# Kernel tuning notes

Hardware: AMD Instinct MI355X
Metric: run time of the kernel (lower is better)

## Reference

```python
import jax, jax.numpy as jnp
import numpy as np

N = 100000
E = 600000
H = 128
EPS = 1e-5


def _layer_norm(x, g, b):
    m = jnp.mean(x, axis=-1, keepdims=True)
    v = jnp.var(x, axis=-1, keepdims=True)
    return (x - m) * jax.lax.rsqrt(v + EPS) * g + b


def _mlp_ln(x, ws, bs, g, b):
    # Linear->ReLU x3, Linear, LayerNorm
    for i in range(4):
        x = x @ ws[i] + bs[i]
        if i < 3:
            x = jax.nn.relu(x)
    return _layer_norm(x, g, b)


def setup_inputs():
    key = jax.random.key(0)
    ks = jax.random.split(key, 32)

    def w(k, i, o):
        return jax.random.normal(k, (i, o), jnp.float32) * (1.0 / np.sqrt(i))

    inp = {
        "node_attr": jax.random.normal(ks[0], (N, H), jnp.float32),
        "edge_attr": jax.random.normal(ks[1], (E, H), jnp.float32),
        "edge_index": jax.random.randint(ks[2], (2, E), 0, N, jnp.int32),
        "num_nodes": N,
        # edge MLP: 3H -> H -> H -> H -> H, LayerNorm(H)
        "ew0": w(ks[3], 3 * H, H), "eb0": jnp.zeros((H,), jnp.float32),
        "ew1": w(ks[4], H, H),     "eb1": jnp.zeros((H,), jnp.float32),
        "ew2": w(ks[5], H, H),     "eb2": jnp.zeros((H,), jnp.float32),
        "ew3": w(ks[6], H, H),     "eb3": jnp.zeros((H,), jnp.float32),
        "eg": jnp.ones((H,), jnp.float32), "ebt": jnp.zeros((H,), jnp.float32),
        # node MLP: 2H -> H -> H -> H -> H, LayerNorm(H)
        "nw0": w(ks[7], 2 * H, H), "nb0": jnp.zeros((H,), jnp.float32),
        "nw1": w(ks[8], H, H),     "nb1": jnp.zeros((H,), jnp.float32),
        "nw2": w(ks[9], H, H),     "nb2": jnp.zeros((H,), jnp.float32),
        "nw3": w(ks[10], H, H),    "nb3": jnp.zeros((H,), jnp.float32),
        "ng": jnp.ones((H,), jnp.float32), "nbt": jnp.zeros((H,), jnp.float32),
    }
    return inp


def reference(node_attr, edge_attr, edge_index, num_nodes,
              ew0, eb0, ew1, eb1, ew2, eb2, ew3, eb3, eg, ebt,
              nw0, nb0, nw1, nb1, nw2, nb2, nw3, nb3, ng, nbt):
    senders, receivers = edge_index[0], edge_index[1]

    # EdgeBlock: gather, concat, MLP+LN
    collected_edges = jnp.concatenate(
        [node_attr[senders], node_attr[receivers], edge_attr], axis=1)  # [E, 3H]
    updated_edge = _mlp_ln(collected_edges, [ew0, ew1, ew2, ew3],
                           [eb0, eb1, eb2, eb3], eg, ebt)  # [E, H]

    # NodeBlock: scatter_add over receivers, concat, MLP+LN
    agg = jax.ops.segment_sum(updated_edge, receivers, num_segments=num_nodes)  # [N, H]
    collected_nodes = jnp.concatenate([node_attr, agg], axis=-1)  # [N, 2H]
    updated_node = _mlp_ln(collected_nodes, [nw0, nw1, nw2, nw3],
                           [nb0, nb1, nb2, nb3], ng, nbt)  # [N, H]

    # residual connections
    return (updated_node + node_attr, updated_edge + edge_attr)
```

## Files before the change

### kernel.cpp

```cpp
#include <hip/hip_runtime.h>

#define HN 128
#define NNODES 100000
#define NEDGES 600000

typedef __attribute__((ext_vector_type(8))) short short8;
typedef __attribute__((ext_vector_type(4))) float f32x4;

__device__ __forceinline__ unsigned short f2bf(float x) {
    unsigned u = __float_as_uint(x);
    u += 0x7FFFu + ((u >> 16) & 1u);
    return (unsigned short)(u >> 16);
}
__device__ __forceinline__ float bf2f(unsigned short h) {
    return __uint_as_float(((unsigned)h) << 16);
}

__device__ __forceinline__ f32x4 mfma16(short8 a, short8 b, f32x4 c) {
    return __builtin_amdgcn_mfma_f32_16x16x32_bf16(a, b, c, 0, 0, 0);
}

__device__ __forceinline__ void split_frag(const float xs[8], short8 &hi, short8 &lo) {
    #pragma unroll
    for (int e = 0; e < 8; ++e) {
        unsigned short h = f2bf(xs[e]);
        hi[e] = (short)h;
        lo[e] = (short)f2bf(xs[e] - bf2f(h));
    }
}

__device__ __forceinline__ void load_frags_global(const float* __restrict__ row,
                                                  short8 ahi[4], short8 alo[4], int g) {
    #pragma unroll
    for (int t = 0; t < 4; ++t) {
        float4 v0 = *(const float4*)(row + 32*t + 8*g);
        float4 v1 = *(const float4*)(row + 32*t + 8*g + 4);
        float xs[8] = {v0.x, v0.y, v0.z, v0.w, v1.x, v1.y, v1.z, v1.w};
        split_frag(xs, ahi[t], alo[t]);
    }
}

__device__ __forceinline__ void mlp_layer2(f32x4 C[2][8],
                                           const short8 ahi[2][4], const short8 alo[2][4],
                                           const unsigned short* __restrict__ Whi,
                                           const unsigned short* __restrict__ Wlo,
                                           int mat, int lane) {
    #pragma unroll
    for (int t = 0; t < 4; ++t) {
        #pragma unroll
        for (int n = 0; n < 8; ++n) {
            size_t idx = ((size_t)((mat*32 + t*8 + n)*64 + lane)) * 8;
            short8 bh = *(const short8*)(Whi + idx);
            short8 bl = *(const short8*)(Wlo + idx);
            #pragma unroll
            for (int i = 0; i < 2; ++i) {
                f32x4 a = C[i][n];
                a = mfma16(ahi[i][t], bh, a);
                a = mfma16(ahi[i][t], bl, a);
                a = mfma16(alo[i][t], bh, a);
                C[i][n] = a;
            }
        }
    }
}

__device__ __forceinline__ void c_to_lds(float* buf, const f32x4 C[8], int g, int c) {
    #pragma unroll
    for (int n = 0; n < 8; ++n) {
        #pragma unroll
        for (int j = 0; j < 4; ++j) {
            int row = 4*g + j;
            int col = 16*n + c;
            buf[(row*HN + col) ^ ((row & 7) << 2)] = C[n][j];
        }
    }
}
__device__ __forceinline__ void lds_to_frags(const float* buf, short8 ahi[4], short8 alo[4],
                                             int g, int c) {
    #pragma unroll
    for (int t = 0; t < 4; ++t) {
        int w0 = c*HN + 32*t + 8*g;
        int x  = (c & 7) << 2;
        float4 v0 = *(const float4*)(buf + (w0 ^ x));
        float4 v1 = *(const float4*)(buf + ((w0 + 4) ^ x));
        float xs[8] = {v0.x, v0.y, v0.z, v0.w, v1.x, v1.y, v1.z, v1.w};
        split_frag(xs, ahi[t], alo[t]);
    }
}

__device__ __forceinline__ void add_bias_act(f32x4 C[8], const float* __restrict__ b,
                                             int c, bool do_relu) {
    #pragma unroll
    for (int n = 0; n < 8; ++n) {
        float bv = b[16*n + c];
        #pragma unroll
        for (int j = 0; j < 4; ++j) {
            float v = C[n][j] + bv;
            C[n][j] = do_relu ? fmaxf(v, 0.0f) : v;
        }
    }
}

__device__ __forceinline__ void apply_ln(f32x4 C[8], const float* __restrict__ gamma,
                                         const float* __restrict__ beta, int c) {
    float s1[4] = {0.f,0.f,0.f,0.f}, s2[4] = {0.f,0.f,0.f,0.f};
    #pragma unroll
    for (int n = 0; n < 8; ++n)
        #pragma unroll
        for (int j = 0; j < 4; ++j) { float v = C[n][j]; s1[j] += v; s2[j] += v*v; }
    #pragma unroll
    for (int m = 1; m < 16; m <<= 1) {
        #pragma unroll
        for (int j = 0; j < 4; ++j) {
            s1[j] += __shfl_xor(s1[j], m);
            s2[j] += __shfl_xor(s2[j], m);
        }
    }
    float mn[4], rs[4];
    #pragma unroll
    for (int j = 0; j < 4; ++j) {
        mn[j] = s1[j] * (1.0f/128.0f);
        float var = s2[j] * (1.0f/128.0f) - mn[j]*mn[j];
        rs[j] = rsqrtf(var + 1e-5f);
    }
    #pragma unroll
    for (int n = 0; n < 8; ++n) {
        float ga = gamma[16*n + c], be = beta[16*n + c];
        #pragma unroll
        for (int j = 0; j < 4; ++j)
            C[n][j] = (C[n][j] - mn[j]) * rs[j] * ga + be;
    }
}

__global__ void prep_weights(const float* __restrict__ ew0, const float* __restrict__ ew1,
                             const float* __restrict__ ew2, const float* __restrict__ ew3,
                             const float* __restrict__ nw0, const float* __restrict__ nw1,
                             const float* __restrict__ nw2, const float* __restrict__ nw3,
                             unsigned short* __restrict__ Whi, unsigned short* __restrict__ Wlo) {
    int gid = blockIdx.x * blockDim.x + threadIdx.x;
    if (gid >= 11*2048) return;
    int lane = gid & 63;
    int n = (gid >> 6) & 7;
    int t = (gid >> 9) & 3;
    int m = gid >> 11;
    const float* src; int roff = 0;
    switch (m) {
        case 0: src = ew0; roff = 256; break;
        case 1: src = ew1; break;
        case 2: src = ew2; break;
        case 3: src = ew3; break;
        case 4: src = nw0; roff = 128; break;
        case 5: src = nw1; break;
        case 6: src = nw2; break;
        case 7: src = nw3; break;
        case 8: src = ew0; roff = 0; break;
        case 9: src = ew0; roff = 128; break;
        default: src = nw0; roff = 0; break;
    }
    int col = 16*n + (lane & 15);
    int rbase = roff + 32*t + 8*(lane >> 4);
    size_t o = (size_t)gid * 8;
    #pragma unroll
    for (int e = 0; e < 8; ++e) {
        float x = src[(size_t)(rbase + e) * HN + col];
        unsigned short h = f2bf(x);
        Whi[o + e] = h;
        Wlo[o + e] = f2bf(x - bf2f(h));
    }
}

__global__ __launch_bounds__(256, 2)
void pre_kernel(const float* __restrict__ na, const float* __restrict__ eb0,
                const float* __restrict__ nb0,
                const unsigned short* __restrict__ Whi, const unsigned short* __restrict__ Wlo,
                float* __restrict__ Ps, float* __restrict__ Pr, float* __restrict__ Pn) {
    int w = threadIdx.x >> 6, lane = threadIdx.x & 63;
    int g = lane >> 4, c = lane & 15;
    int n0 = (blockIdx.x * 4 + w) * 32;
    if (n0 >= NNODES) return;

    short8 ahi[2][4], alo[2][4];
    load_frags_global(na + (size_t)(n0 + c) * HN, ahi[0], alo[0], g);
    load_frags_global(na + (size_t)(n0 + 16 + c) * HN, ahi[1], alo[1], g);

    #pragma unroll
    for (int mi = 0; mi < 3; ++mi) {
        f32x4 acc[2][8];
        #pragma unroll
        for (int i = 0; i < 2; ++i)
            #pragma unroll
            for (int n = 0; n < 8; ++n) acc[i][n] = (f32x4){0.f, 0.f, 0.f, 0.f};
        mlp_layer2(acc, ahi, alo, Whi, Wlo, 8 + mi, lane);
        float* dst = (mi == 0) ? Ps : (mi == 1) ? Pr : Pn;
        #pragma unroll
        for (int n = 0; n < 8; ++n) {
            int col = 16*n + c;
            float bv = (mi == 0) ? eb0[col] : (mi == 2) ? nb0[col] : 0.0f;
            #pragma unroll
            for (int i = 0; i < 2; ++i)
                #pragma unroll
                for (int j = 0; j < 4; ++j) {
                    size_t row = (size_t)(n0 + 16*i + 4*g + j);
                    dst[row*HN + col] = acc[i][n][j] + bv;
                }
        }
    }
}

__global__ __launch_bounds__(256, 2)
void edge_kernel(const float* __restrict__ ea, const int* __restrict__ eidx,
                 const float* __restrict__ Ps, const float* __restrict__ Pr,
                 const unsigned short* __restrict__ Whi, const unsigned short* __restrict__ Wlo,
                 const float* __restrict__ eb1, const float* __restrict__ eb2,
                 const float* __restrict__ eb3, const float* __restrict__ eg,
                 const float* __restrict__ ebt,
                 float* __restrict__ agg, float* __restrict__ out) {
    __shared__ float xp[4 * 16 * HN];
    int w = threadIdx.x >> 6, lane = threadIdx.x & 63;
    int g = lane >> 4, c = lane & 15;
    int e0 = (blockIdx.x * 4 + w) * 32;
    if (e0 >= NEDGES) return;
    float* buf = xp + w * (16 * HN);
    const int* senders = eidx;
    const int* receivers = eidx + NEDGES;

    short8 ahi[2][4], alo[2][4];
    load_frags_global(ea + (size_t)(e0 + c) * HN, ahi[0], alo[0], g);
    load_frags_global(ea + (size_t)(e0 + 16 + c) * HN, ahi[1], alo[1], g);

    f32x4 C[2][8];
    #pragma unroll
    for (int i = 0; i < 2; ++i)
        #pragma unroll
        for (int n = 0; n < 8; ++n) C[i][n] = (f32x4){0.f, 0.f, 0.f, 0.f};

    mlp_layer2(C, ahi, alo, Whi, Wlo, 0, lane);

    int sid[2][4], rid[2][4];
    #pragma unroll
    for (int i = 0; i < 2; ++i)
        #pragma unroll
        for (int j = 0; j < 4; ++j) {
            int e = e0 + 16*i + 4*g + j;
            sid[i][j] = senders[e];
            rid[i][j] = receivers[e];
        }
    #pragma unroll
    for (int n = 0; n < 8; ++n) {
        int col = 16*n + c;
        #pragma unroll
        for (int i = 0; i < 2; ++i)
            #pragma unroll
            for (int j = 0; j < 4; ++j)
                C[i][n][j] = fmaxf(C[i][n][j] + Ps[(size_t)sid[i][j]*HN + col]
                                              + Pr[(size_t)rid[i][j]*HN + col], 0.0f);
    }
    #pragma unroll
    for (int i = 0; i < 2; ++i) {
        c_to_lds(buf, C[i], g, c);
        lds_to_frags(buf, ahi[i], alo[i], g, c);
    }

    #pragma unroll
    for (int L = 1; L <= 2; ++L) {
        #pragma unroll
        for (int i = 0; i < 2; ++i)
            #pragma unroll
            for (int n = 0; n < 8; ++n) C[i][n] = (f32x4){0.f, 0.f, 0.f, 0.f};
        mlp_layer2(C, ahi, alo, Whi, Wlo, L, lane);
        #pragma unroll
        for (int i = 0; i < 2; ++i) {
            add_bias_act(C[i], (L == 1) ? eb1 : eb2, c, true);
            c_to_lds(buf, C[i], g, c);
            lds_to_frags(buf, ahi[i], alo[i], g, c);
        }
    }

    #pragma unroll
    for (int i = 0; i < 2; ++i)
        #pragma unroll
        for (int n = 0; n < 8; ++n) C[i][n] = (f32x4){0.f, 0.f, 0.f, 0.f};
    mlp_layer2(C, ahi, alo, Whi, Wlo, 3, lane);
    #pragma unroll
    for (int i = 0; i < 2; ++i) {
        add_bias_act(C[i], eb3, c, false);
        apply_ln(C[i], eg, ebt, c);
    }

    #pragma unroll
    for (int n = 0; n < 8; ++n) {
        int col = 16*n + c;
        #pragma unroll
        for (int i = 0; i < 2; ++i)
            #pragma unroll
            for (int j = 0; j < 4; ++j) {
                size_t e = (size_t)(e0 + 16*i + 4*g + j);
                float v = C[i][n][j];
                unsafeAtomicAdd(&agg[(size_t)rid[i][j]*HN + col], v);
                out[((size_t)NNODES + e)*HN + col] = v + ea[e*HN + col];
            }
    }
}

__global__ __launch_bounds__(256, 2)
void node_kernel(const float* __restrict__ na, const float* __restrict__ agg,
                 const float* __restrict__ Pn,
                 const unsigned short* __restrict__ Whi, const unsigned short* __restrict__ Wlo,
                 const float* __restrict__ nb1, const float* __restrict__ nb2,
                 const float* __restrict__ nb3, const float* __restrict__ ng,
                 const float* __restrict__ nbt,
                 float* __restrict__ out) {
    __shared__ float xp[4 * 16 * HN];
    int w = threadIdx.x >> 6, lane = threadIdx.x & 63;
    int g = lane >> 4, c = lane & 15;
    int n0 = (blockIdx.x * 4 + w) * 32;
    if (n0 >= NNODES) return;
    float* buf = xp + w * (16 * HN);

    short8 ahi[2][4], alo[2][4];
    load_frags_global(agg + (size_t)(n0 + c) * HN, ahi[0], alo[0], g);
    load_frags_global(agg + (size_t)(n0 + 16 + c) * HN, ahi[1], alo[1], g);

    f32x4 C[2][8];
    #pragma unroll
    for (int i = 0; i < 2; ++i)
        #pragma unroll
        for (int n = 0; n < 8; ++n) C[i][n] = (f32x4){0.f, 0.f, 0.f, 0.f};

    mlp_layer2(C, ahi, alo, Whi, Wlo, 4, lane);
    #pragma unroll
    for (int n = 0; n < 8; ++n) {
        int col = 16*n + c;
        #pragma unroll
        for (int i = 0; i < 2; ++i)
            #pragma unroll
            for (int j = 0; j < 4; ++j)
                C[i][n][j] = fmaxf(C[i][n][j] + Pn[(size_t)(n0 + 16*i + 4*g + j)*HN + col], 0.0f);
    }
    #pragma unroll
    for (int i = 0; i < 2; ++i) {
        c_to_lds(buf, C[i], g, c);
        lds_to_frags(buf, ahi[i], alo[i], g, c);
    }

    #pragma unroll
    for (int L = 5; L <= 6; ++L) {
        #pragma unroll
        for (int i = 0; i < 2; ++i)
            #pragma unroll
            for (int n = 0; n < 8; ++n) C[i][n] = (f32x4){0.f, 0.f, 0.f, 0.f};
        mlp_layer2(C, ahi, alo, Whi, Wlo, L, lane);
        #pragma unroll
        for (int i = 0; i < 2; ++i) {
            add_bias_act(C[i], (L == 5) ? nb1 : nb2, c, true);
            c_to_lds(buf, C[i], g, c);
            lds_to_frags(buf, ahi[i], alo[i], g, c);
        }
    }

    #pragma unroll
    for (int i = 0; i < 2; ++i)
        #pragma unroll
        for (int n = 0; n < 8; ++n) C[i][n] = (f32x4){0.f, 0.f, 0.f, 0.f};
    mlp_layer2(C, ahi, alo, Whi, Wlo, 7, lane);
    #pragma unroll
    for (int i = 0; i < 2; ++i) {
        add_bias_act(C[i], nb3, c, false);
        apply_ln(C[i], ng, nbt, c);
    }

    #pragma unroll
    for (int n = 0; n < 8; ++n) {
        int col = 16*n + c;
        #pragma unroll
        for (int i = 0; i < 2; ++i)
            #pragma unroll
            for (int j = 0; j < 4; ++j) {
                size_t row = (size_t)(n0 + 16*i + 4*g + j);
                out[row*HN + col] = C[i][n][j] + na[row*HN + col];
            }
    }
}

extern "C" void kernel_launch(void* const* d_in, const int* in_sizes, int n_in,
                              void* d_out, int out_size, void* d_ws, size_t ws_size,
                              hipStream_t stream) {
    const float* node_attr = (const float*)d_in[0];
    const float* edge_attr = (const float*)d_in[1];
    const int*   edge_index = (const int*)d_in[2];
    const float* ew0 = (const float*)d_in[4];
    const float* eb0 = (const float*)d_in[5];
    const float* ew1 = (const float*)d_in[6];
    const float* eb1 = (const float*)d_in[7];
    const float* ew2 = (const float*)d_in[8];
    const float* eb2 = (const float*)d_in[9];
    const float* ew3 = (const float*)d_in[10];
    const float* eb3 = (const float*)d_in[11];
    const float* eg  = (const float*)d_in[12];
    const float* ebt = (const float*)d_in[13];
    const float* nw0 = (const float*)d_in[14];
    const float* nb0 = (const float*)d_in[15];
    const float* nw1 = (const float*)d_in[16];
    const float* nb1 = (const float*)d_in[17];
    const float* nw2 = (const float*)d_in[18];
    const float* nb2 = (const float*)d_in[19];
    const float* nw3 = (const float*)d_in[20];
    const float* nb3 = (const float*)d_in[21];
    const float* ng  = (const float*)d_in[22];
    const float* nbt = (const float*)d_in[23];
    float* out = (float*)d_out;

    const size_t NH = (size_t)NNODES * HN * sizeof(float);
    char* ws = (char*)d_ws;
    float* agg = (float*)(ws);
    float* Ps  = (float*)(ws + NH);
    float* Pr  = (float*)(ws + 2*NH);
    float* Pn  = (float*)(ws + 3*NH);
    unsigned short* Whi = (unsigned short*)(ws + 4*NH);
    unsigned short* Wlo = Whi + (size_t)11 * 2048 * 8;

    hipMemsetAsync(agg, 0, NH, stream);
    prep_weights<<<88, 256, 0, stream>>>(ew0, ew1, ew2, ew3, nw0, nw1, nw2, nw3, Whi, Wlo);

    int preWaves  = NNODES / 32;
    int edgeWaves = NEDGES / 32;
    int nodeWaves = NNODES / 32;
    pre_kernel<<<(preWaves + 3)/4, 256, 0, stream>>>(node_attr, eb0, nb0, Whi, Wlo, Ps, Pr, Pn);
    edge_kernel<<<(edgeWaves + 3)/4, 256, 0, stream>>>(edge_attr, edge_index, Ps, Pr, Whi, Wlo,
                                                       eb1, eb2, eb3, eg, ebt, agg, out);
    node_kernel<<<(nodeWaves + 3)/4, 256, 0, stream>>>(node_attr, agg, Pn, Whi, Wlo,
                                                       nb1, nb2, nb3, ng, nbt, out);
}
```

Before: 1.678 ms.

## Shrink per-wave tile to 16 rows and raise occupancy to three blocks

Each wave now handles 16 rows instead of 32 in all three kernels, which halves the accumulator and fragment register footprint. Launch bounds go from 2 to 3 blocks per CU to exploit the freed registers. The weight loads for each k-step are batched before the MFMAs, and the edge gather of Ps/Pr is split into two batches of loads. The trade-off is that each weight fragment is reused across only one 16-row tile, so weight traffic per row doubles, in exchange for more latency hiding on the random gathers and atomics.

After: 1.520 ms. 1.1x faster.

```diff
diff --git a/kernel.cpp b/kernel.cpp
--- a/kernel.cpp
+++ b/kernel.cpp
@@ -40,26 +40,26 @@
     }
 }
 
-__device__ __forceinline__ void mlp_layer2(f32x4 C[2][8],
-                                           const short8 ahi[2][4], const short8 alo[2][4],
-                                           const unsigned short* __restrict__ Whi,
-                                           const unsigned short* __restrict__ Wlo,
-                                           int mat, int lane) {
+__device__ __forceinline__ void mlp_layer16(f32x4 C[8], const short8 ahi[4], const short8 alo[4],
+                                            const unsigned short* __restrict__ Whi,
+                                            const unsigned short* __restrict__ Wlo,
+                                            int mat, int lane) {
     #pragma unroll
     for (int t = 0; t < 4; ++t) {
+        short8 bh[8], bl[8];
         #pragma unroll
         for (int n = 0; n < 8; ++n) {
             size_t idx = ((size_t)((mat*32 + t*8 + n)*64 + lane)) * 8;
-            short8 bh = *(const short8*)(Whi + idx);
-            short8 bl = *(const short8*)(Wlo + idx);
-            #pragma unroll
-            for (int i = 0; i < 2; ++i) {
-                f32x4 a = C[i][n];
-                a = mfma16(ahi[i][t], bh, a);
-                a = mfma16(ahi[i][t], bl, a);
-                a = mfma16(alo[i][t], bh, a);
-                C[i][n] = a;
-            }
+            bh[n] = *(const short8*)(Whi + idx);
+            bl[n] = *(const short8*)(Wlo + idx);
+        }
+        #pragma unroll
+        for (int n = 0; n < 8; ++n) {
+            f32x4 a = C[n];
+            a = mfma16(ahi[t], bh[n], a);
+            a = mfma16(ahi[t], bl[n], a);
+            a = mfma16(alo[t], bh[n], a);
+            C[n] = a;
         }
     }
 }
@@ -169,45 +169,38 @@
     }
 }
 
-__global__ __launch_bounds__(256, 2)
+__global__ __launch_bounds__(256, 3)
 void pre_kernel(const float* __restrict__ na, const float* __restrict__ eb0,
                 const float* __restrict__ nb0,
                 const unsigned short* __restrict__ Whi, const unsigned short* __restrict__ Wlo,
                 float* __restrict__ Ps, float* __restrict__ Pr, float* __restrict__ Pn) {
     int w = threadIdx.x >> 6, lane = threadIdx.x & 63;
     int g = lane >> 4, c = lane & 15;
-    int n0 = (blockIdx.x * 4 + w) * 32;
+    int n0 = (blockIdx.x * 4 + w) * 16;
     if (n0 >= NNODES) return;
 
-    short8 ahi[2][4], alo[2][4];
-    load_frags_global(na + (size_t)(n0 + c) * HN, ahi[0], alo[0], g);
-    load_frags_global(na + (size_t)(n0 + 16 + c) * HN, ahi[1], alo[1], g);
+    short8 ahi[4], alo[4];
+    load_frags_global(na + (size_t)(n0 + c) * HN, ahi, alo, g);
 
     #pragma unroll
     for (int mi = 0; mi < 3; ++mi) {
-        f32x4 acc[2][8];
-        #pragma unroll
-        for (int i = 0; i < 2; ++i)
-            #pragma unroll
-            for (int n = 0; n < 8; ++n) acc[i][n] = (f32x4){0.f, 0.f, 0.f, 0.f};
-        mlp_layer2(acc, ahi, alo, Whi, Wlo, 8 + mi, lane);
+        f32x4 acc[8];
+        #pragma unroll
+        for (int n = 0; n < 8; ++n) acc[n] = (f32x4){0.f, 0.f, 0.f, 0.f};
+        mlp_layer16(acc, ahi, alo, Whi, Wlo, 8 + mi, lane);
         float* dst = (mi == 0) ? Ps : (mi == 1) ? Pr : Pn;
         #pragma unroll
         for (int n = 0; n < 8; ++n) {
             int col = 16*n + c;
             float bv = (mi == 0) ? eb0[col] : (mi == 2) ? nb0[col] : 0.0f;
             #pragma unroll
-            for (int i = 0; i < 2; ++i)
-                #pragma unroll
-                for (int j = 0; j < 4; ++j) {
-                    size_t row = (size_t)(n0 + 16*i + 4*g + j);
-                    dst[row*HN + col] = acc[i][n][j] + bv;
-                }
-        }
-    }
-}
-
-__global__ __launch_bounds__(256, 2)
+            for (int j = 0; j < 4; ++j)
+                dst[(size_t)(n0 + 4*g + j)*HN + col] = acc[n][j] + bv;
+        }
+    }
+}
+
+__global__ __launch_bounds__(256, 3)
 void edge_kernel(const float* __restrict__ ea, const int* __restrict__ eidx,
                  const float* __restrict__ Ps, const float* __restrict__ Pr,
                  const unsigned short* __restrict__ Whi, const unsigned short* __restrict__ Wlo,
@@ -218,91 +211,80 @@
     __shared__ float xp[4 * 16 * HN];
     int w = threadIdx.x >> 6, lane = threadIdx.x & 63;
     int g = lane >> 4, c = lane & 15;
-    int e0 = (blockIdx.x * 4 + w) * 32;
+    int e0 = (blockIdx.x * 4 + w) * 16;
     if (e0 >= NEDGES) return;
     float* buf = xp + w * (16 * HN);
     const int* senders = eidx;
     const int* receivers = eidx + NEDGES;
 
-    short8 ahi[2][4], alo[2][4];
-    load_frags_global(ea + (size_t)(e0 + c) * HN, ahi[0], alo[0], g);
-    load_frags_global(ea + (size_t)(e0 + 16 + c) * HN, ahi[1], alo[1], g);
-
-    f32x4 C[2][8];
-    #pragma unroll
-    for (int i = 0; i < 2; ++i)
-        #pragma unroll
-        for (int n = 0; n < 8; ++n) C[i][n] = (f32x4){0.f, 0.f, 0.f, 0.f};
-
-    mlp_layer2(C, ahi, alo, Whi, Wlo, 0, lane);
-
-    int sid[2][4], rid[2][4];
-    #pragma unroll
-    for (int i = 0; i < 2; ++i)
-        #pragma unroll
-        for (int j = 0; j < 4; ++j) {
-            int e = e0 + 16*i + 4*g + j;
-            sid[i][j] = senders[e];
-            rid[i][j] = receivers[e];
-        }
-    #pragma unroll
-    for (int n = 0; n < 8; ++n) {
-        int col = 16*n + c;
-        #pragma unroll
-        for (int i = 0; i < 2; ++i)
-            #pragma unroll
-            for (int j = 0; j < 4; ++j)
-                C[i][n][j] = fmaxf(C[i][n][j] + Ps[(size_t)sid[i][j]*HN + col]
-                                              + Pr[(size_t)rid[i][j]*HN + col], 0.0f);
-    }
-    #pragma unroll
-    for (int i = 0; i < 2; ++i) {
-        c_to_lds(buf, C[i], g, c);
-        lds_to_frags(buf, ahi[i], alo[i], g, c);
-    }
-
-    #pragma unroll
-    for (int L = 1; L <= 2; ++L) {
-        #pragma unroll
-        for (int i = 0; i < 2; ++i)
-            #pragma unroll
-            for (int n = 0; n < 8; ++n) C[i][n] = (f32x4){0.f, 0.f, 0.f, 0.f};
-        mlp_layer2(C, ahi, alo, Whi, Wlo, L, lane);
-        #pragma unroll
-        for (int i = 0; i < 2; ++i) {
-            add_bias_act(C[i], (L == 1) ? eb1 : eb2, c, true);
-            c_to_lds(buf, C[i], g, c);
-            lds_to_frags(buf, ahi[i], alo[i], g, c);
-        }
-    }
-
-    #pragma unroll
-    for (int i = 0; i < 2; ++i)
-        #pragma unroll
-        for (int n = 0; n < 8; ++n) C[i][n] = (f32x4){0.f, 0.f, 0.f, 0.f};
-    mlp_layer2(C, ahi, alo, Whi, Wlo, 3, lane);
-    #pragma unroll
-    for (int i = 0; i < 2; ++i) {
-        add_bias_act(C[i], eb3, c, false);
-        apply_ln(C[i], eg, ebt, c);
-    }
-
-    #pragma unroll
-    for (int n = 0; n < 8; ++n) {
-        int col = 16*n + c;
-        #pragma unroll
-        for (int i = 0; i < 2; ++i)
+    short8 ahi[4], alo[4];
+    load_frags_global(ea + (size_t)(e0 + c) * HN, ahi, alo, g);
+
+    int sid[4], rid[4];
+    #pragma unroll
+    for (int j = 0; j < 4; ++j) {
+        int e = e0 + 4*g + j;
+        sid[j] = senders[e];
+        rid[j] = receivers[e];
+    }
+
+    f32x4 C[8];
+    #pragma unroll
+    for (int n = 0; n < 8; ++n) C[n] = (f32x4){0.f, 0.f, 0.f, 0.f};
+
+    mlp_layer16(C, ahi, alo, Whi, Wlo, 0, lane);
+
+    #pragma unroll
+    for (int nh = 0; nh < 2; ++nh) {
+        float pv[16];
+        #pragma unroll
+        for (int n = 0; n < 4; ++n)
             #pragma unroll
             for (int j = 0; j < 4; ++j) {
-                size_t e = (size_t)(e0 + 16*i + 4*g + j);
-                float v = C[i][n][j];
-                unsafeAtomicAdd(&agg[(size_t)rid[i][j]*HN + col], v);
-                out[((size_t)NNODES + e)*HN + col] = v + ea[e*HN + col];
+                int col = 16*(4*nh + n) + c;
+                pv[n*4 + j] = Ps[(size_t)sid[j]*HN + col] + Pr[(size_t)rid[j]*HN + col];
             }
-    }
-}
-
-__global__ __launch_bounds__(256, 2)
+        #pragma unroll
+        for (int n = 0; n < 4; ++n)
+            #pragma unroll
+            for (int j = 0; j < 4; ++j) {
+                int nn = 4*nh + n;
+                C[nn][j] = fmaxf(C[nn][j] + pv[n*4 + j], 0.0f);
+            }
+    }
+    c_to_lds(buf, C, g, c);
+    lds_to_frags(buf, ahi, alo, g, c);
+
+    #pragma unroll
+    for (int L = 1; L <= 2; ++L) {
+        #pragma unroll
+        for (int n = 0; n < 8; ++n) C[n] = (f32x4){0.f, 0.f, 0.f, 0.f};
+        mlp_layer16(C, ahi, alo, Whi, Wlo, L, lane);
+        add_bias_act(C, (L == 1) ? eb1 : eb2, c, true);
+        c_to_lds(buf, C, g, c);
+        lds_to_frags(buf, ahi, alo, g, c);
+    }
+
+    #pragma unroll
+    for (int n = 0; n < 8; ++n) C[n] = (f32x4){0.f, 0.f, 0.f, 0.f};
+    mlp_layer16(C, ahi, alo, Whi, Wlo, 3, lane);
+    add_bias_act(C, eb3, c, false);
+    apply_ln(C, eg, ebt, c);
+
+    #pragma unroll
+    for (int n = 0; n < 8; ++n) {
+        int col = 16*n + c;
+        #pragma unroll
+        for (int j = 0; j < 4; ++j) {
+            size_t e = (size_t)(e0 + 4*g + j);
+            float v = C[n][j];
+            unsafeAtomicAdd(&agg[(size_t)rid[j]*HN + col], v);
+            out[((size_t)NNODES + e)*HN + col] = v + ea[e*HN + col];
+        }
+    }
+}
+
+__global__ __launch_bounds__(256, 3)
 void node_kernel(const float* __restrict__ na, const float* __restrict__ agg,
                  const float* __restrict__ Pn,
                  const unsigned short* __restrict__ Whi, const unsigned short* __restrict__ Wlo,
@@ -313,72 +295,52 @@
     __shared__ float xp[4 * 16 * HN];
     int w = threadIdx.x >> 6, lane = threadIdx.x & 63;
     int g = lane >> 4, c = lane & 15;
-    int n0 = (blockIdx.x * 4 + w) * 32;
+    int n0 = (blockIdx.x * 4 + w) * 16;
     if (n0 >= NNODES) return;
     float* buf = xp + w * (16 * HN);
 
-    short8 ahi[2][4], alo[2][4];
-    load_frags_global(agg + (size_t)(n0 + c) * HN, ahi[0], alo[0], g);
-    load_frags_global(agg + (size_t)(n0 + 16 + c) * HN, ahi[1], alo[1], g);
-
-    f32x4 C[2][8];
-    #pragma unroll
-    for (int i = 0; i < 2; ++i)
-        #pragma unroll
-        for (int n = 0; n < 8; ++n) C[i][n] = (f32x4){0.f, 0.f, 0.f, 0.f};
-
-    mlp_layer2(C, ahi, alo, Whi, Wlo, 4, lane);
+    short8 ahi[4], alo[4];
+    load_frags_global(agg + (size_t)(n0 + c) * HN, ahi, alo, g);
+
+    f32x4 C[8];
+    #pragma unroll
+    for (int n = 0; n < 8; ++n) C[n] = (f32x4){0.f, 0.f, 0.f, 0.f};
+
+    mlp_layer16(C, ahi, alo, Whi, Wlo, 4, lane);
     #pragma unroll
     for (int n = 0; n < 8; ++n) {
         int col = 16*n + c;
         #pragma unroll
-        for (int i = 0; i < 2; ++i)
-            #pragma unroll
-            for (int j = 0; j < 4; ++j)
-                C[i][n][j] = fmaxf(C[i][n][j] + Pn[(size_t)(n0 + 16*i + 4*g + j)*HN + col], 0.0f);
-    }
-    #pragma unroll
-    for (int i = 0; i < 2; ++i) {
-        c_to_lds(buf, C[i], g, c);
-        lds_to_frags(buf, ahi[i], alo[i], g, c);
-    }
+        for (int j = 0; j < 4; ++j)
+            C[n][j] = fmaxf(C[n][j] + Pn[(size_t)(n0 + 4*g + j)*HN + col], 0.0f);
+    }
+    c_to_lds(buf, C, g, c);
+    lds_to_frags(buf, ahi, alo, g, c);
 
     #pragma unroll
     for (int L = 5; L <= 6; ++L) {
         #pragma unroll
-        for (int i = 0; i < 2; ++i)
-            #pragma unroll
-            for (int n = 0; n < 8; ++n) C[i][n] = (f32x4){0.f, 0.f, 0.f, 0.f};
-        mlp_layer2(C, ahi, alo, Whi, Wlo, L, lane);
-        #pragma unroll
-        for (int i = 0; i < 2; ++i) {
-            add_bias_act(C[i], (L == 5) ? nb1 : nb2, c, true);
-            c_to_lds(buf, C[i], g, c);
-            lds_to_frags(buf, ahi[i], alo[i], g, c);
-        }
-    }
-
-    #pragma unroll
-    for (int i = 0; i < 2; ++i)
-        #pragma unroll
-        for (int n = 0; n < 8; ++n) C[i][n] = (f32x4){0.f, 0.f, 0.f, 0.f};
-    mlp_layer2(C, ahi, alo, Whi, Wlo, 7, lane);
-    #pragma unroll
-    for (int i = 0; i < 2; ++i) {
-        add_bias_act(C[i], nb3, c, false);
-        apply_ln(C[i], ng, nbt, c);
-    }
+        for (int n = 0; n < 8; ++n) C[n] = (f32x4){0.f, 0.f, 0.f, 0.f};
+        mlp_layer16(C, ahi, alo, Whi, Wlo, L, lane);
+        add_bias_act(C, (L == 5) ? nb1 : nb2, c, true);
+        c_to_lds(buf, C, g, c);
+        lds_to_frags(buf, ahi, alo, g, c);
+    }
+
+    #pragma unroll
+    for (int n = 0; n < 8; ++n) C[n] = (f32x4){0.f, 0.f, 0.f, 0.f};
+    mlp_layer16(C, ahi, alo, Whi, Wlo, 7, lane);
+    add_bias_act(C, nb3, c, false);
+    apply_ln(C, ng, nbt, c);
 
     #pragma unroll
     for (int n = 0; n < 8; ++n) {
         int col = 16*n + c;
         #pragma unroll
-        for (int i = 0; i < 2; ++i)
-            #pragma unroll
-            for (int j = 0; j < 4; ++j) {
-                size_t row = (size_t)(n0 + 16*i + 4*g + j);
-                out[row*HN + col] = C[i][n][j] + na[row*HN + col];
-            }
+        for (int j = 0; j < 4; ++j) {
+            size_t row = (size_t)(n0 + 4*g + j);
+            out[row*HN + col] = C[n][j] + na[row*HN + col];
+        }
     }
 }
 
@@ -422,12 +384,11 @@
     hipMemsetAsync(agg, 0, NH, stream);
     prep_weights<<<88, 256, 0, stream>>>(ew0, ew1, ew2, ew3, nw0, nw1, nw2, nw3, Whi, Wlo);
 
-    int preWaves  = NNODES / 32;
-    int edgeWaves = NEDGES / 32;
-    int nodeWaves = NNODES / 32;
+    int preWaves  = NNODES / 16;
+    int edgeWaves = NEDGES / 16;
     pre_kernel<<<(preWaves + 3)/4, 256, 0, stream>>>(node_attr, eb0, nb0, Whi, Wlo, Ps, Pr, Pn);
     edge_kernel<<<(edgeWaves + 3)/4, 256, 0, stream>>>(edge_attr, edge_index, Ps, Pr, Whi, Wlo,
                                                        eb1, eb2, eb3, eg, ebt, agg, out);
-    node_kernel<<<(nodeWaves + 3)/4, 256, 0, stream>>>(node_attr, agg, Pn, Whi, Wlo,
-                                                       nb1, nb2, nb3, ng, nbt, out);
-}
+    node_kernel<<<(preWaves + 3)/4, 256, 0, stream>>>(node_attr, agg, Pn, Whi, Wlo,
+                                                      nb1, nb2, nb3, ng, nbt, out);
+}
```
